# Kernel optimization log

Measured on AMD Instinct MI355X. Metric: run time of the kernel, lower is better.

Reference implementation:

```python
import jax, jax.numpy as jnp
import numpy as np

B, C, N = 4, 192, 4096
K = 16                      # avg degree
E = B * N * K               # 262144 edges
C_OUT = 384


def setup_inputs() -> dict:
    key = jax.random.key(0)
    k1, k2, k3, k4 = jax.random.split(key, 4)
    x = jax.random.normal(k1, (B, C, N, 1), dtype=jnp.float32)
    edge_index = jax.random.randint(k2, (2, E), 0, B * N, dtype=jnp.int64)
    # BasicConv([2C, C_OUT]): 1x1 Conv2d + bias + ReLU (norm=None)
    W = jax.random.normal(k3, (C_OUT, 2 * C), dtype=jnp.float32) * (1.0 / np.sqrt(2 * C))
    b = jax.random.normal(k4, (C_OUT,), dtype=jnp.float32) * 0.01
    return {"x": x, "edge_index": edge_index, "W": W, "b": b}


def reference(x, edge_index, W, b):
    Bs, Cs, Ns, _ = x.shape
    BN = Bs * Ns
    # (B,C,N,1) -> flattened node table (B*N, C); node id = b*N + n
    x_flat = jnp.transpose(x[..., 0], (0, 2, 1)).reshape(BN, Cs)
    x_i = x_flat[edge_index[0]]          # (E, C) gather at dst
    x_j = x_flat[edge_index[1]]          # (E, C) gather at src
    diff = x_j - x_i
    # scatter-max over dst nodes; torch_scatter fills empty segments with 0
    agg = jax.ops.segment_max(diff, edge_index[0], num_segments=BN)
    agg = jnp.where(jnp.isfinite(agg), agg, 0.0)
    x_j_out = jnp.transpose(agg.reshape(Bs, Ns, Cs), (0, 2, 1))[..., None]  # (B,C,N,1)
    # interleave channels: cat along new axis 2 then reshape -> (B, 2C, N, 1)
    cat = jnp.stack([x, x_j_out], axis=2).reshape(Bs, 2 * Cs, Ns, 1)
    # 1x1 conv == GEMM over channels, + bias + ReLU
    out = jnp.einsum('oc,bcnw->bonw', W, cat) + b[None, :, None, None]
    return jax.nn.relu(out)
```

## Files before the change

### kernel.cpp

```cpp
#include <hip/hip_runtime.h>
#include <hip/hip_bf16.h>
#include <math.h>

#define Bz    4
#define Cch   192
#define Nn    4096
#define BN    16384
#define Ecnt  262144
#define COUT  384
#define CAP   64
#define MSTR  200

typedef __attribute__((ext_vector_type(8))) short short8;
typedef __attribute__((ext_vector_type(4))) float floatx4;

__device__ __forceinline__ void gload_lds16(const void* g, void* l) {
    __builtin_amdgcn_global_load_lds(
        (const __attribute__((address_space(1))) unsigned int*)g,
        (__attribute__((address_space(3))) unsigned int*)l, 16, 0, 0);
}

__device__ __forceinline__ float b2f(unsigned short u) {
    union { unsigned int i; float f; } z; z.i = ((unsigned int)u) << 16; return z.f;
}
__device__ __forceinline__ unsigned short f2b(float f) {
    __hip_bfloat16 h = __float2bfloat16(f);
    return *(unsigned short*)&h;
}

__global__ __launch_bounds__(256) void prep_kernel(
    const float* __restrict__ x, const unsigned int* __restrict__ ew,
    const float* __restrict__ W, __hip_bfloat16* __restrict__ xb,
    __hip_bfloat16* __restrict__ Wxa, __hip_bfloat16* __restrict__ Wa,
    int* __restrict__ deg, int* __restrict__ flag) {
    int bid = blockIdx.x;
    if (bid < 3072) {
        __shared__ float tile[32][33];
        int b = bid / 768;
        int r = bid - b * 768;
        int c0 = (r >> 7) * 32;
        int n0 = (r & 127) * 32;
        int tx = threadIdx.x & 31, ty = threadIdx.x >> 5;
        for (int i = ty; i < 32; i += 8)
            tile[i][tx] = x[((size_t)(b * Cch + c0 + i)) * Nn + n0 + tx];
        __syncthreads();
        for (int i = ty; i < 32; i += 8)
            xb[((size_t)(b * Nn + n0 + i)) * Cch + c0 + tx] =
                __float2bfloat16(tile[tx][i]);
    } else if (bid < 3360) {
        int i = (bid - 3072) * 256 + threadIdx.x;
        int o = i / Cch, c = i - o * Cch;
        float wx = W[o * 2 * Cch + 2 * c];
        float wa = W[o * 2 * Cch + 2 * c + 1];
        Wxa[i] = __float2bfloat16(wx - wa);
        Wa[i]  = __float2bfloat16(wa);
    } else if (bid < 3424) {
        deg[(bid - 3360) * 256 + threadIdx.x] = 0;
    } else {
        __shared__ int s;
        if (threadIdx.x == 0) s = 1;
        __syncthreads();
        if (ew[2 * threadIdx.x + 1] != 0u) atomicAnd(&s, 0);
        __syncthreads();
        if (threadIdx.x == 0) *flag = s;
    }
}

__global__ __launch_bounds__(256) void fill_kernel(
    const int* __restrict__ ew, const int* __restrict__ flag,
    int* __restrict__ deg, int* __restrict__ slots) {
    int t = blockIdx.x * 256 + threadIdx.x;
    int d0, d1, s0, s1;
    if (*flag) {
        int4 dv = *(const int4*)&ew[4 * t];
        int4 sv = *(const int4*)&ew[2 * Ecnt + 4 * t];
        d0 = dv.x; d1 = dv.z; s0 = sv.x; s1 = sv.z;
    } else {
        int2 dv = *(const int2*)&ew[2 * t];
        int2 sv = *(const int2*)&ew[Ecnt + 2 * t];
        d0 = dv.x; d1 = dv.y; s0 = sv.x; s1 = sv.y;
    }
    int p0 = atomicAdd(&deg[d0], 1); if (p0 < CAP) slots[(d0 << 6) + p0] = s0;
    int p1 = atomicAdd(&deg[d1], 1); if (p1 < CAP) slots[(d1 << 6) + p1] = s1;
}

#define RED8(mm, FLD) do {                                                    \
    float a_ = fmaxf(fmaxf(b2f(v[0].FLD), b2f(v[1].FLD)),                     \
                     fmaxf(b2f(v[2].FLD), b2f(v[3].FLD)));                    \
    float b_ = fmaxf(fmaxf(b2f(v[4].FLD), b2f(v[5].FLD)),                     \
                     fmaxf(b2f(v[6].FLD), b2f(v[7].FLD)));                    \
    mm = fmaxf(mm, fmaxf(a_, b_)); } while (0)

__global__ __launch_bounds__(256) void fused_kernel(
    const int* __restrict__ deg, const int* __restrict__ slots,
    const __hip_bfloat16* __restrict__ xb,
    const __hip_bfloat16* __restrict__ Wxa, const __hip_bfloat16* __restrict__ Wa,
    const float* __restrict__ bias, float* __restrict__ out) {
    __shared__ unsigned short Ms[32 * MSTR];
    __shared__ short As[2][128 * 8];
    __shared__ short Bs[2][1536 * 8];
    int t = threadIdx.x;
    int lane = t & 63, wave = t >> 6;
    int quad = lane >> 4, lrow = lane & 15;
    int node0 = blockIdx.x * 32;
    const unsigned short* xbu = (const unsigned short*)xb;

    auto STAGE = [&](int skt, int bf_) {
        const __hip_bfloat16* Wseg = (skt >= 6) ? Wa : Wxa;
        int kt = ((skt >= 6) ? skt - 6 : skt) * 32;
#pragma unroll
        for (int m = 0; m < 6; m++) {
            int o = m * 64 + lane;
            gload_lds16(Wseg + (size_t)o * Cch + kt + wave * 8,
                        &Bs[bf_][(wave * 384 + o) * 8]);
        }
        if (skt < 6 && wave < 2) {
            int c = wave * 64 + lane;
            int q = c >> 5, nd = c & 31;
            gload_lds16(xb + (size_t)(node0 + nd) * Cch + kt + q * 8,
                        &As[bf_][c * 8]);
        }
    };

    STAGE(0, 0);

    int act = lane < 48;
    int cb = lane * 4;
    for (int nl = wave * 8; nl < wave * 8 + 8; nl++) {
        int node = node0 + nl;
        int d = deg[node]; if (d > CAP) d = CAP;
        d = __builtin_amdgcn_readfirstlane(d);
        int nbrval = 0;
        if (lane < d) nbrval = slots[(node << 6) + lane];
        float m0 = -INFINITY, m1 = -INFINITY, m2 = -INFINITY, m3 = -INFINITY;
        int k = 0;
        for (; k + 8 <= d; k += 8) {
            int s[8];
#pragma unroll
            for (int u = 0; u < 8; u++) s[u] = __builtin_amdgcn_readlane(nbrval, k + u);
            if (act) {
                ushort4 v[8];
#pragma unroll
                for (int u = 0; u < 8; u++) v[u] = *(const ushort4*)&xbu[s[u] * Cch + cb];
                RED8(m0, x); RED8(m1, y); RED8(m2, z); RED8(m3, w);
            }
        }
        if (k + 4 <= d) {
            int s0 = __builtin_amdgcn_readlane(nbrval, k);
            int s1 = __builtin_amdgcn_readlane(nbrval, k + 1);
            int s2 = __builtin_amdgcn_readlane(nbrval, k + 2);
            int s3 = __builtin_amdgcn_readlane(nbrval, k + 3);
            if (act) {
                ushort4 v0 = *(const ushort4*)&xbu[s0 * Cch + cb];
                ushort4 v1 = *(const ushort4*)&xbu[s1 * Cch + cb];
                ushort4 v2 = *(const ushort4*)&xbu[s2 * Cch + cb];
                ushort4 v3 = *(const ushort4*)&xbu[s3 * Cch + cb];
                m0 = fmaxf(m0, fmaxf(fmaxf(b2f(v0.x), b2f(v1.x)), fmaxf(b2f(v2.x), b2f(v3.x))));
                m1 = fmaxf(m1, fmaxf(fmaxf(b2f(v0.y), b2f(v1.y)), fmaxf(b2f(v2.y), b2f(v3.y))));
                m2 = fmaxf(m2, fmaxf(fmaxf(b2f(v0.z), b2f(v1.z)), fmaxf(b2f(v2.z), b2f(v3.z))));
                m3 = fmaxf(m3, fmaxf(fmaxf(b2f(v0.w), b2f(v1.w)), fmaxf(b2f(v2.w), b2f(v3.w))));
            }
            k += 4;
        }
        for (; k < d; k++) {
            int s = __builtin_amdgcn_readlane(nbrval, k);
            if (act) {
                ushort4 v = *(const ushort4*)&xbu[s * Cch + cb];
                m0 = fmaxf(m0, b2f(v.x)); m1 = fmaxf(m1, b2f(v.y));
                m2 = fmaxf(m2, b2f(v.z)); m3 = fmaxf(m3, b2f(v.w));
            }
        }
        if (act) {
            ushort4 o4;
            if (d > 0) {
                o4.x = f2b(m0); o4.y = f2b(m1); o4.z = f2b(m2); o4.w = f2b(m3);
            } else {
                o4 = *(const ushort4*)&xbu[node * Cch + cb];
            }
            *(ushort4*)&Ms[nl * MSTR + cb] = o4;
        }
    }
    __syncthreads();

    floatx4 acc[2][6] = {};
    for (int s = 0; s < 12; s++) {
        int p = s & 1;
        if (s < 11) STAGE(s + 1, p ^ 1);
        short8 af[2], bf[6];
        if (s < 6) {
#pragma unroll
            for (int i = 0; i < 2; i++)
                af[i] = *(const short8*)&As[p][(quad * 32 + i * 16 + lrow) * 8];
        } else {
            int kk = (s - 6) * 32 + quad * 8;
#pragma unroll
            for (int i = 0; i < 2; i++)
                af[i] = *(const short8*)&Ms[(i * 16 + lrow) * MSTR + kk];
        }
#pragma unroll
        for (int j = 0; j < 6; j++)
            bf[j] = *(const short8*)&Bs[p][(quad * 384 + wave * 96 + j * 16 + lrow) * 8];
#pragma unroll
        for (int i = 0; i < 2; i++)
#pragma unroll
            for (int j = 0; j < 6; j++)
                acc[i][j] = __builtin_amdgcn_mfma_f32_16x16x32_bf16(bf[j], af[i], acc[i][j], 0, 0, 0);
        __syncthreads();
    }

#pragma unroll
    for (int i = 0; i < 2; i++) {
        int node = node0 + i * 16 + lrow;
        int b = node >> 12, n = node & 4095;
#pragma unroll
        for (int j = 0; j < 6; j++) {
            int ob = wave * 96 + j * 16 + quad * 4;
#pragma unroll
            for (int r = 0; r < 4; r++) {
                int o = ob + r;
                float v = acc[i][j][r] + bias[o];
                out[((size_t)(b * COUT + o)) * Nn + n] = fmaxf(v, 0.0f);
            }
        }
    }
}

extern "C" void kernel_launch(void* const* d_in, const int* in_sizes, int n_in,
                              void* d_out, int out_size, void* d_ws, size_t ws_size,
                              hipStream_t stream) {
    const float* x    = (const float*)d_in[0];
    const int*   ew   = (const int*)d_in[1];
    const float* W    = (const float*)d_in[2];
    const float* bias = (const float*)d_in[3];
    float* out        = (float*)d_out;

    char* ws = (char*)d_ws;
    __hip_bfloat16* xb   = (__hip_bfloat16*)ws;
    __hip_bfloat16* Wxa  = (__hip_bfloat16*)(ws + 12582912);
    __hip_bfloat16* Wa   = (__hip_bfloat16*)(ws + 12730368);
    int* deg   = (int*)(ws + 12877824);
    int* slots = (int*)(ws + 12943360);
    int* flag  = (int*)(ws + 17137664);

    prep_kernel<<<3425, 256, 0, stream>>>(x, (const unsigned int*)ew, W, xb, Wxa, Wa, deg, flag);
    fill_kernel<<<Ecnt / 512, 256, 0, stream>>>(ew, flag, deg, slots);
    fused_kernel<<<BN / 32, 256, 0, stream>>>(deg, slots, xb, Wxa, Wa, bias, out);
}
```

Baseline: 135.5 us.

## Merge three kernels into one cooperative persistent kernel with grid syncs

Replaces the three separate launches (prep, CSR fill, fused gather-max+GEMM) with a single cooperative kernel of 512 blocks x 512 threads, separated by grid-wide syncs, and keeps a three-kernel fallback if the cooperative launch fails. The GEMM phase now reads weights directly from global memory instead of double-buffered LDS staging, stages the node's own features into LDS during the gather loop, and halves per-wave output tiles to 8 waves per block. The aim is to remove launch gaps and inter-kernel drain, at the cost of grid-sync overhead, no global-to-LDS prefetch pipelining, and a fixed grid that must fit co-resident.

```diff
diff --git a/kernel.cpp b/kernel.cpp
--- a/kernel.cpp
+++ b/kernel.cpp
@@ -1,5 +1,6 @@
 #include <hip/hip_runtime.h>
 #include <hip/hip_bf16.h>
+#include <hip/hip_cooperative_groups.h>
 #include <math.h>
 
 #define Bz    4
@@ -10,15 +11,11 @@
 #define COUT  384
 #define CAP   64
 #define MSTR  200
+#define NBLK  512
+#define NTHR  512
 
 typedef __attribute__((ext_vector_type(8))) short short8;
 typedef __attribute__((ext_vector_type(4))) float floatx4;
-
-__device__ __forceinline__ void gload_lds16(const void* g, void* l) {
-    __builtin_amdgcn_global_load_lds(
-        (const __attribute__((address_space(1))) unsigned int*)g,
-        (__attribute__((address_space(3))) unsigned int*)l, 16, 0, 0);
-}
 
 __device__ __forceinline__ float b2f(unsigned short u) {
     union { unsigned int i; float f; } z; z.i = ((unsigned int)u) << 16; return z.f;
@@ -26,62 +23,6 @@
 __device__ __forceinline__ unsigned short f2b(float f) {
     __hip_bfloat16 h = __float2bfloat16(f);
     return *(unsigned short*)&h;
-}
-
-__global__ __launch_bounds__(256) void prep_kernel(
-    const float* __restrict__ x, const unsigned int* __restrict__ ew,
-    const float* __restrict__ W, __hip_bfloat16* __restrict__ xb,
-    __hip_bfloat16* __restrict__ Wxa, __hip_bfloat16* __restrict__ Wa,
-    int* __restrict__ deg, int* __restrict__ flag) {
-    int bid = blockIdx.x;
-    if (bid < 3072) {
-        __shared__ float tile[32][33];
-        int b = bid / 768;
-        int r = bid - b * 768;
-        int c0 = (r >> 7) * 32;
-        int n0 = (r & 127) * 32;
-        int tx = threadIdx.x & 31, ty = threadIdx.x >> 5;
-        for (int i = ty; i < 32; i += 8)
-            tile[i][tx] = x[((size_t)(b * Cch + c0 + i)) * Nn + n0 + tx];
-        __syncthreads();
-        for (int i = ty; i < 32; i += 8)
-            xb[((size_t)(b * Nn + n0 + i)) * Cch + c0 + tx] =
-                __float2bfloat16(tile[tx][i]);
-    } else if (bid < 3360) {
-        int i = (bid - 3072) * 256 + threadIdx.x;
-        int o = i / Cch, c = i - o * Cch;
-        float wx = W[o * 2 * Cch + 2 * c];
-        float wa = W[o * 2 * Cch + 2 * c + 1];
-        Wxa[i] = __float2bfloat16(wx - wa);
-        Wa[i]  = __float2bfloat16(wa);
-    } else if (bid < 3424) {
-        deg[(bid - 3360) * 256 + threadIdx.x] = 0;
-    } else {
-        __shared__ int s;
-        if (threadIdx.x == 0) s = 1;
-        __syncthreads();
-        if (ew[2 * threadIdx.x + 1] != 0u) atomicAnd(&s, 0);
-        __syncthreads();
-        if (threadIdx.x == 0) *flag = s;
-    }
-}
-
-__global__ __launch_bounds__(256) void fill_kernel(
-    const int* __restrict__ ew, const int* __restrict__ flag,
-    int* __restrict__ deg, int* __restrict__ slots) {
-    int t = blockIdx.x * 256 + threadIdx.x;
-    int d0, d1, s0, s1;
-    if (*flag) {
-        int4 dv = *(const int4*)&ew[4 * t];
-        int4 sv = *(const int4*)&ew[2 * Ecnt + 4 * t];
-        d0 = dv.x; d1 = dv.z; s0 = sv.x; s1 = sv.z;
-    } else {
-        int2 dv = *(const int2*)&ew[2 * t];
-        int2 sv = *(const int2*)&ew[Ecnt + 2 * t];
-        d0 = dv.x; d1 = dv.y; s0 = sv.x; s1 = sv.y;
-    }
-    int p0 = atomicAdd(&deg[d0], 1); if (p0 < CAP) slots[(d0 << 6) + p0] = s0;
-    int p1 = atomicAdd(&deg[d1], 1); if (p1 < CAP) slots[(d1 << 6) + p1] = s1;
 }
 
 #define RED8(mm, FLD) do {                                                    \
@@ -91,47 +32,85 @@
                      fmaxf(b2f(v[6].FLD), b2f(v[7].FLD)));                    \
     mm = fmaxf(mm, fmaxf(a_, b_)); } while (0)
 
-__global__ __launch_bounds__(256) void fused_kernel(
+
+__device__ __forceinline__ void p0_body(
+    int bid, int tid, void* smem,
+    const float* __restrict__ x, const unsigned int* __restrict__ ew,
+    const float* __restrict__ W, __hip_bfloat16* __restrict__ xb,
+    __hip_bfloat16* __restrict__ Wxa, __hip_bfloat16* __restrict__ Wa,
+    int* __restrict__ deg, int* __restrict__ flag)
+{
+    float (*tr)[33] = (float(*)[33])smem;
+    int tx = tid & 31, ty = tid >> 5;
+    for (int r = bid; r < 3072; r += NBLK) {
+        int b = r / 768, rr = r - b * 768;
+        int c0 = (rr >> 7) * 32, n0 = (rr & 127) * 32;
+        for (int i = ty; i < 32; i += 16)
+            tr[i][tx] = x[((size_t)(b * Cch + c0 + i)) * Nn + n0 + tx];
+        __syncthreads();
+        for (int i = ty; i < 32; i += 16)
+            xb[((size_t)(b * Nn + n0 + i)) * Cch + c0 + tx] =
+                __float2bfloat16(tr[tx][i]);
+        __syncthreads();
+    }
+    int idx = bid * NTHR + tid;
+    if (idx < COUT * Cch) {
+        int o = idx / Cch, c = idx - o * Cch;
+        float wx = W[o * 2 * Cch + 2 * c];
+        float wa = W[o * 2 * Cch + 2 * c + 1];
+        Wxa[idx] = __float2bfloat16(wx - wa);
+        Wa[idx]  = __float2bfloat16(wa);
+    }
+    if (idx < BN) deg[idx] = 0;
+    if (bid == 0) {
+        if (tid == 0) *flag = 1;
+        __syncthreads();
+        if (ew[2 * tid + 1] != 0u) atomicAnd(flag, 0);
+    }
+}
+
+__device__ __forceinline__ void p1_body(
+    int bid, int tid, const unsigned int* __restrict__ ew,
+    const int* __restrict__ flag, int* __restrict__ deg,
+    int* __restrict__ slots)
+{
+    int t = bid * NTHR + tid;
+    int d0, s0;
+    if (*flag) {
+        d0 = (int)ew[2 * t];
+        s0 = (int)ew[2 * Ecnt + 2 * t];
+    } else {
+        d0 = (int)ew[t];
+        s0 = (int)ew[Ecnt + t];
+    }
+    int p0 = atomicAdd(&deg[d0], 1);
+    if (p0 < CAP) slots[(d0 << 6) + p0] = s0;
+}
+
+__device__ __forceinline__ void p2_body(
+    int bid, int tid, void* smem,
     const int* __restrict__ deg, const int* __restrict__ slots,
     const __hip_bfloat16* __restrict__ xb,
     const __hip_bfloat16* __restrict__ Wxa, const __hip_bfloat16* __restrict__ Wa,
-    const float* __restrict__ bias, float* __restrict__ out) {
-    __shared__ unsigned short Ms[32 * MSTR];
-    __shared__ short As[2][128 * 8];
-    __shared__ short Bs[2][1536 * 8];
-    int t = threadIdx.x;
-    int lane = t & 63, wave = t >> 6;
+    const float* __restrict__ bias, float* __restrict__ out)
+{
+    unsigned short* Xs = (unsigned short*)smem;
+    unsigned short* Ms = (unsigned short*)((char*)smem + 32 * MSTR * 2);
+    int lane = tid & 63, wave = tid >> 6;
     int quad = lane >> 4, lrow = lane & 15;
-    int node0 = blockIdx.x * 32;
+    int node0 = bid * 32;
     const unsigned short* xbu = (const unsigned short*)xb;
-
-    auto STAGE = [&](int skt, int bf_) {
-        const __hip_bfloat16* Wseg = (skt >= 6) ? Wa : Wxa;
-        int kt = ((skt >= 6) ? skt - 6 : skt) * 32;
-#pragma unroll
-        for (int m = 0; m < 6; m++) {
-            int o = m * 64 + lane;
-            gload_lds16(Wseg + (size_t)o * Cch + kt + wave * 8,
-                        &Bs[bf_][(wave * 384 + o) * 8]);
-        }
-        if (skt < 6 && wave < 2) {
-            int c = wave * 64 + lane;
-            int q = c >> 5, nd = c & 31;
-            gload_lds16(xb + (size_t)(node0 + nd) * Cch + kt + q * 8,
-                        &As[bf_][c * 8]);
-        }
-    };
-
-    STAGE(0, 0);
-
     int act = lane < 48;
     int cb = lane * 4;
-    for (int nl = wave * 8; nl < wave * 8 + 8; nl++) {
+
+    for (int nl = wave * 4; nl < wave * 4 + 4; nl++) {
         int node = node0 + nl;
         int d = deg[node]; if (d > CAP) d = CAP;
         d = __builtin_amdgcn_readfirstlane(d);
         int nbrval = 0;
         if (lane < d) nbrval = slots[(node << 6) + lane];
+        ushort4 xv = {0, 0, 0, 0};
+        if (act) xv = *(const ushort4*)&xbu[node * Cch + cb];
         float m0 = -INFINITY, m1 = -INFINITY, m2 = -INFINITY, m3 = -INFINITY;
         int k = 0;
         for (; k + 8 <= d; k += 8) {
@@ -171,41 +150,50 @@
             }
         }
         if (act) {
+            *(ushort4*)&Xs[nl * MSTR + cb] = xv;
             ushort4 o4;
             if (d > 0) {
                 o4.x = f2b(m0); o4.y = f2b(m1); o4.z = f2b(m2); o4.w = f2b(m3);
             } else {
-                o4 = *(const ushort4*)&xbu[node * Cch + cb];
+                o4 = xv;
             }
             *(ushort4*)&Ms[nl * MSTR + cb] = o4;
         }
     }
     __syncthreads();
 
-    floatx4 acc[2][6] = {};
-    for (int s = 0; s < 12; s++) {
-        int p = s & 1;
-        if (s < 11) STAGE(s + 1, p ^ 1);
-        short8 af[2], bf[6];
-        if (s < 6) {
-#pragma unroll
-            for (int i = 0; i < 2; i++)
-                af[i] = *(const short8*)&As[p][(quad * 32 + i * 16 + lrow) * 8];
-        } else {
-            int kk = (s - 6) * 32 + quad * 8;
-#pragma unroll
-            for (int i = 0; i < 2; i++)
-                af[i] = *(const short8*)&Ms[(i * 16 + lrow) * MSTR + kk];
-        }
-#pragma unroll
-        for (int j = 0; j < 6; j++)
-            bf[j] = *(const short8*)&Bs[p][(quad * 384 + wave * 96 + j * 16 + lrow) * 8];
-#pragma unroll
-        for (int i = 0; i < 2; i++)
-#pragma unroll
-            for (int j = 0; j < 6; j++)
+    floatx4 acc[2][3] = {};
+    const unsigned short* Wx16 = (const unsigned short*)Wxa;
+    const unsigned short* Wa16 = (const unsigned short*)Wa;
+    for (int s = 0; s < 6; s++) {
+        int kk = s * 32 + quad * 8;
+        short8 af[2], bf[3];
+#pragma unroll
+        for (int i = 0; i < 2; i++)
+            af[i] = *(const short8*)&Xs[(i * 16 + lrow) * MSTR + kk];
+#pragma unroll
+        for (int j = 0; j < 3; j++)
+            bf[j] = *(const short8*)&Wx16[(size_t)(wave * 48 + j * 16 + lrow) * Cch + kk];
+#pragma unroll
+        for (int i = 0; i < 2; i++)
+#pragma unroll
+            for (int j = 0; j < 3; j++)
                 acc[i][j] = __builtin_amdgcn_mfma_f32_16x16x32_bf16(bf[j], af[i], acc[i][j], 0, 0, 0);
-        __syncthreads();
+    }
+    for (int s = 0; s < 6; s++) {
+        int kk = s * 32 + quad * 8;
+        short8 af[2], bf[3];
+#pragma unroll
+        for (int i = 0; i < 2; i++)
+            af[i] = *(const short8*)&Ms[(i * 16 + lrow) * MSTR + kk];
+#pragma unroll
+        for (int j = 0; j < 3; j++)
+            bf[j] = *(const short8*)&Wa16[(size_t)(wave * 48 + j * 16 + lrow) * Cch + kk];
+#pragma unroll
+        for (int i = 0; i < 2; i++)
+#pragma unroll
+            for (int j = 0; j < 3; j++)
+                acc[i][j] = __builtin_amdgcn_mfma_f32_16x16x32_bf16(bf[j], af[i], acc[i][j], 0, 0, 0);
     }
 
 #pragma unroll
@@ -213,8 +201,8 @@
         int node = node0 + i * 16 + lrow;
         int b = node >> 12, n = node & 4095;
 #pragma unroll
-        for (int j = 0; j < 6; j++) {
-            int ob = wave * 96 + j * 16 + quad * 4;
+        for (int j = 0; j < 3; j++) {
+            int ob = wave * 48 + j * 16 + quad * 4;
 #pragma unroll
             for (int r = 0; r < 4; r++) {
                 int o = ob + r;
@@ -225,11 +213,53 @@
     }
 }
 
+__global__ __launch_bounds__(NTHR, 4) void mono_kernel(
+    const float* __restrict__ x, const unsigned int* __restrict__ ew,
+    const float* __restrict__ W, const float* __restrict__ bias,
+    __hip_bfloat16* __restrict__ xb, __hip_bfloat16* __restrict__ Wxa,
+    __hip_bfloat16* __restrict__ Wa, int* __restrict__ deg,
+    int* __restrict__ slots, int* __restrict__ flag,
+    float* __restrict__ out)
+{
+    __shared__ __align__(16) char smem[2 * 32 * MSTR * 2];
+    int tid = threadIdx.x, bid = blockIdx.x;
+    p0_body(bid, tid, smem, x, ew, W, xb, Wxa, Wa, deg, flag);
+    cooperative_groups::this_grid().sync();
+    p1_body(bid, tid, ew, flag, deg, slots);
+    cooperative_groups::this_grid().sync();
+    p2_body(bid, tid, smem, deg, slots, xb, Wxa, Wa, bias, out);
+}
+
+__global__ __launch_bounds__(NTHR) void p0_kernel(
+    const float* __restrict__ x, const unsigned int* __restrict__ ew,
+    const float* __restrict__ W, __hip_bfloat16* __restrict__ xb,
+    __hip_bfloat16* __restrict__ Wxa, __hip_bfloat16* __restrict__ Wa,
+    int* __restrict__ deg, int* __restrict__ flag)
+{
+    __shared__ __align__(16) char smem[4224];
+    p0_body(blockIdx.x, threadIdx.x, smem, x, ew, W, xb, Wxa, Wa, deg, flag);
+}
+__global__ __launch_bounds__(NTHR) void p1_kernel(
+    const unsigned int* __restrict__ ew, const int* __restrict__ flag,
+    int* __restrict__ deg, int* __restrict__ slots)
+{
+    p1_body(blockIdx.x, threadIdx.x, ew, flag, deg, slots);
+}
+__global__ __launch_bounds__(NTHR, 4) void p2_kernel(
+    const int* __restrict__ deg, const int* __restrict__ slots,
+    const __hip_bfloat16* __restrict__ xb,
+    const __hip_bfloat16* __restrict__ Wxa, const __hip_bfloat16* __restrict__ Wa,
+    const float* __restrict__ bias, float* __restrict__ out)
+{
+    __shared__ __align__(16) char smem[2 * 32 * MSTR * 2];
+    p2_body(blockIdx.x, threadIdx.x, smem, deg, slots, xb, Wxa, Wa, bias, out);
+}
+
 extern "C" void kernel_launch(void* const* d_in, const int* in_sizes, int n_in,
                               void* d_out, int out_size, void* d_ws, size_t ws_size,
                               hipStream_t stream) {
     const float* x    = (const float*)d_in[0];
-    const int*   ew   = (const int*)d_in[1];
+    const unsigned int* ew = (const unsigned int*)d_in[1];
     const float* W    = (const float*)d_in[2];
     const float* bias = (const float*)d_in[3];
     float* out        = (float*)d_out;
@@ -242,7 +272,15 @@
     int* slots = (int*)(ws + 12943360);
     int* flag  = (int*)(ws + 17137664);
 
-    prep_kernel<<<3425, 256, 0, stream>>>(x, (const unsigned int*)ew, W, xb, Wxa, Wa, deg, flag);
-    fill_kernel<<<Ecnt / 512, 256, 0, stream>>>(ew, flag, deg, slots);
-    fused_kernel<<<BN / 32, 256, 0, stream>>>(deg, slots, xb, Wxa, Wa, bias, out);
-}
+    void* args[] = { (void*)&x, (void*)&ew, (void*)&W, (void*)&bias,
+                     (void*)&xb, (void*)&Wxa, (void*)&Wa, (void*)&deg,
+                     (void*)&slots, (void*)&flag, (void*)&out };
+    hipError_t err = hipLaunchCooperativeKernel((const void*)mono_kernel,
+                                                dim3(NBLK), dim3(NTHR),
+                                                args, 0, stream);
+    if (err != hipSuccess) {
+        p0_kernel<<<NBLK, NTHR, 0, stream>>>(x, ew, W, xb, Wxa, Wa, deg, flag);
+        p1_kernel<<<NBLK, NTHR, 0, stream>>>(ew, flag, deg, slots);
+        p2_kernel<<<NBLK, NTHR, 0, stream>>>(deg, slots, xb, Wxa, Wa, bias, out);
+    }
+}
```

New measurement: 262.2 us. 93.5% more time.

## Use 512-thread blocks with register-prefetched weights instead of LDS staging

Applied to the files above, without the earlier changes.

The fused gather-max plus GEMM kernel now runs 8 waves per block. Each wave handles 4 nodes in the gather phase and 48 output channels in the GEMM. The double-buffered LDS staging of weights via global_load_lds is replaced by per-wave direct global loads of W fragments into registers, prefetched one k-step ahead. The per-step barriers are gone, and the node's own features are kept in LDS instead of being restaged. This aims to cut LDS traffic and sync overhead and raise occupancy, at the cost of redundant global weight reads across blocks that now rely on L2.

```diff
diff --git a/kernel.cpp b/kernel.cpp
--- a/kernel.cpp
+++ b/kernel.cpp
@@ -14,12 +14,6 @@
 typedef __attribute__((ext_vector_type(8))) short short8;
 typedef __attribute__((ext_vector_type(4))) float floatx4;
 
-__device__ __forceinline__ void gload_lds16(const void* g, void* l) {
-    __builtin_amdgcn_global_load_lds(
-        (const __attribute__((address_space(1))) unsigned int*)g,
-        (__attribute__((address_space(3))) unsigned int*)l, 16, 0, 0);
-}
-
 __device__ __forceinline__ float b2f(unsigned short u) {
     union { unsigned int i; float f; } z; z.i = ((unsigned int)u) << 16; return z.f;
 }
@@ -27,6 +21,13 @@
     __hip_bfloat16 h = __float2bfloat16(f);
     return *(unsigned short*)&h;
 }
+
+#define RED8(mm, FLD) do {                                                    \
+    float a_ = fmaxf(fmaxf(b2f(v[0].FLD), b2f(v[1].FLD)),                     \
+                     fmaxf(b2f(v[2].FLD), b2f(v[3].FLD)));                    \
+    float b_ = fmaxf(fmaxf(b2f(v[4].FLD), b2f(v[5].FLD)),                     \
+                     fmaxf(b2f(v[6].FLD), b2f(v[7].FLD)));                    \
+    mm = fmaxf(mm, fmaxf(a_, b_)); } while (0)
 
 __global__ __launch_bounds__(256) void prep_kernel(
     const float* __restrict__ x, const unsigned int* __restrict__ ew,
@@ -84,54 +85,38 @@
     int p1 = atomicAdd(&deg[d1], 1); if (p1 < CAP) slots[(d1 << 6) + p1] = s1;
 }
 
-#define RED8(mm, FLD) do {                                                    \
-    float a_ = fmaxf(fmaxf(b2f(v[0].FLD), b2f(v[1].FLD)),                     \
-                     fmaxf(b2f(v[2].FLD), b2f(v[3].FLD)));                    \
-    float b_ = fmaxf(fmaxf(b2f(v[4].FLD), b2f(v[5].FLD)),                     \
-                     fmaxf(b2f(v[6].FLD), b2f(v[7].FLD)));                    \
-    mm = fmaxf(mm, fmaxf(a_, b_)); } while (0)
-
-__global__ __launch_bounds__(256) void fused_kernel(
+#define MFMA6()                                                                \
+    acc00 = __builtin_amdgcn_mfma_f32_16x16x32_bf16(b0, af0, acc00, 0, 0, 0);  \
+    acc10 = __builtin_amdgcn_mfma_f32_16x16x32_bf16(b0, af1, acc10, 0, 0, 0);  \
+    acc01 = __builtin_amdgcn_mfma_f32_16x16x32_bf16(b1, af0, acc01, 0, 0, 0);  \
+    acc11 = __builtin_amdgcn_mfma_f32_16x16x32_bf16(b1, af1, acc11, 0, 0, 0);  \
+    acc02 = __builtin_amdgcn_mfma_f32_16x16x32_bf16(b2, af0, acc02, 0, 0, 0);  \
+    acc12 = __builtin_amdgcn_mfma_f32_16x16x32_bf16(b2, af1, acc12, 0, 0, 0)
+
+__global__ __launch_bounds__(512, 4) void p2_kernel(
     const int* __restrict__ deg, const int* __restrict__ slots,
     const __hip_bfloat16* __restrict__ xb,
     const __hip_bfloat16* __restrict__ Wxa, const __hip_bfloat16* __restrict__ Wa,
-    const float* __restrict__ bias, float* __restrict__ out) {
-    __shared__ unsigned short Ms[32 * MSTR];
-    __shared__ short As[2][128 * 8];
-    __shared__ short Bs[2][1536 * 8];
-    int t = threadIdx.x;
-    int lane = t & 63, wave = t >> 6;
+    const float* __restrict__ bias, float* __restrict__ out)
+{
+    __shared__ __align__(16) unsigned short Xs[32 * MSTR];
+    __shared__ __align__(16) unsigned short Ms[32 * MSTR];
+    int tid = threadIdx.x, bid = blockIdx.x;
+    int lane = tid & 63, wave = tid >> 6;
     int quad = lane >> 4, lrow = lane & 15;
-    int node0 = blockIdx.x * 32;
+    int node0 = bid * 32;
     const unsigned short* xbu = (const unsigned short*)xb;
-
-    auto STAGE = [&](int skt, int bf_) {
-        const __hip_bfloat16* Wseg = (skt >= 6) ? Wa : Wxa;
-        int kt = ((skt >= 6) ? skt - 6 : skt) * 32;
-#pragma unroll
-        for (int m = 0; m < 6; m++) {
-            int o = m * 64 + lane;
-            gload_lds16(Wseg + (size_t)o * Cch + kt + wave * 8,
-                        &Bs[bf_][(wave * 384 + o) * 8]);
-        }
-        if (skt < 6 && wave < 2) {
-            int c = wave * 64 + lane;
-            int q = c >> 5, nd = c & 31;
-            gload_lds16(xb + (size_t)(node0 + nd) * Cch + kt + q * 8,
-                        &As[bf_][c * 8]);
-        }
-    };
-
-    STAGE(0, 0);
-
     int act = lane < 48;
     int cb = lane * 4;
-    for (int nl = wave * 8; nl < wave * 8 + 8; nl++) {
+
+    for (int nl = wave * 4; nl < wave * 4 + 4; nl++) {
         int node = node0 + nl;
         int d = deg[node]; if (d > CAP) d = CAP;
         d = __builtin_amdgcn_readfirstlane(d);
         int nbrval = 0;
         if (lane < d) nbrval = slots[(node << 6) + lane];
+        ushort4 xv = {0, 0, 0, 0};
+        if (act) xv = *(const ushort4*)&xbu[node * Cch + cb];
         float m0 = -INFINITY, m1 = -INFINITY, m2 = -INFINITY, m3 = -INFINITY;
         int k = 0;
         for (; k + 8 <= d; k += 8) {
@@ -171,54 +156,60 @@
             }
         }
         if (act) {
+            *(ushort4*)&Xs[nl * MSTR + cb] = xv;
             ushort4 o4;
             if (d > 0) {
                 o4.x = f2b(m0); o4.y = f2b(m1); o4.z = f2b(m2); o4.w = f2b(m3);
             } else {
-                o4 = *(const ushort4*)&xbu[node * Cch + cb];
+                o4 = xv;
             }
             *(ushort4*)&Ms[nl * MSTR + cb] = o4;
         }
     }
     __syncthreads();
 
-    floatx4 acc[2][6] = {};
+    floatx4 acc00 = {}, acc01 = {}, acc02 = {}, acc10 = {}, acc11 = {}, acc12 = {};
+    const unsigned short* Wx16 = (const unsigned short*)Wxa;
+    const unsigned short* Wa16 = (const unsigned short*)Wa;
+    size_t w0 = (size_t)(wave * 48 +  0 + lrow) * Cch;
+    size_t w1 = (size_t)(wave * 48 + 16 + lrow) * Cch;
+    size_t w2 = (size_t)(wave * 48 + 32 + lrow) * Cch;
+    int kq = quad * 8;
+
+    short8 b0 = *(const short8*)&Wx16[w0 + kq];
+    short8 b1 = *(const short8*)&Wx16[w1 + kq];
+    short8 b2 = *(const short8*)&Wx16[w2 + kq];
+#pragma unroll
     for (int s = 0; s < 12; s++) {
-        int p = s & 1;
-        if (s < 11) STAGE(s + 1, p ^ 1);
-        short8 af[2], bf[6];
-        if (s < 6) {
-#pragma unroll
-            for (int i = 0; i < 2; i++)
-                af[i] = *(const short8*)&As[p][(quad * 32 + i * 16 + lrow) * 8];
-        } else {
-            int kk = (s - 6) * 32 + quad * 8;
-#pragma unroll
-            for (int i = 0; i < 2; i++)
-                af[i] = *(const short8*)&Ms[(i * 16 + lrow) * MSTR + kk];
-        }
-#pragma unroll
-        for (int j = 0; j < 6; j++)
-            bf[j] = *(const short8*)&Bs[p][(quad * 384 + wave * 96 + j * 16 + lrow) * 8];
-#pragma unroll
-        for (int i = 0; i < 2; i++)
-#pragma unroll
-            for (int j = 0; j < 6; j++)
-                acc[i][j] = __builtin_amdgcn_mfma_f32_16x16x32_bf16(bf[j], af[i], acc[i][j], 0, 0, 0);
-        __syncthreads();
-    }
-
+        short8 n0, n1, n2;
+        if (s < 11) {
+            int sn = s + 1;
+            const unsigned short* Wn = (sn >= 6) ? Wa16 : Wx16;
+            int kkn = ((sn >= 6) ? sn - 6 : sn) * 32 + kq;
+            n0 = *(const short8*)&Wn[w0 + kkn];
+            n1 = *(const short8*)&Wn[w1 + kkn];
+            n2 = *(const short8*)&Wn[w2 + kkn];
+        }
+        int kk = ((s >= 6) ? s - 6 : s) * 32 + kq;
+        const unsigned short* Ar = (s >= 6) ? Ms : Xs;
+        short8 af0 = *(const short8*)&Ar[lrow * MSTR + kk];
+        short8 af1 = *(const short8*)&Ar[(16 + lrow) * MSTR + kk];
+        MFMA6();
+        if (s < 11) { b0 = n0; b1 = n1; b2 = n2; }
+    }
+
+    floatx4 accs[2][3] = {{acc00, acc01, acc02}, {acc10, acc11, acc12}};
 #pragma unroll
     for (int i = 0; i < 2; i++) {
         int node = node0 + i * 16 + lrow;
         int b = node >> 12, n = node & 4095;
 #pragma unroll
-        for (int j = 0; j < 6; j++) {
-            int ob = wave * 96 + j * 16 + quad * 4;
+        for (int j = 0; j < 3; j++) {
+            int ob = wave * 48 + j * 16 + quad * 4;
 #pragma unroll
             for (int r = 0; r < 4; r++) {
                 int o = ob + r;
-                float v = acc[i][j][r] + bias[o];
+                float v = accs[i][j][r] + bias[o];
                 out[((size_t)(b * COUT + o)) * Nn + n] = fmaxf(v, 0.0f);
             }
         }
@@ -244,5 +235,5 @@
 
     prep_kernel<<<3425, 256, 0, stream>>>(x, (const unsigned int*)ew, W, xb, Wxa, Wa, deg, flag);
     fill_kernel<<<Ecnt / 512, 256, 0, stream>>>(ew, flag, deg, slots);
-    fused_kernel<<<BN / 32, 256, 0, stream>>>(deg, slots, xb, Wxa, Wa, bias, out);
-}
+    p2_kernel<<<BN / 32, 512, 0, stream>>>(deg, slots, xb, Wxa, Wa, bias, out);
+}
```

Measured after the change: 123.2 us. 9.1% less time.
